# Performance work log

Hardware: AMD Instinct MI355X
Metric: run time of the kernel (lower is better)

## Reference

```python
import jax, jax.numpy as jnp
import numpy as np

NUM_EMBEDDINGS = 512
EMBEDDING_DIM = 256
COMMITMENT_COST = 0.25


def setup_inputs() -> dict:
    key = jax.random.key(0)
    k1, k2 = jax.random.split(key)
    z_e = jax.random.normal(k1, (16, EMBEDDING_DIM, 16, 16, 16), dtype=jnp.float32)
    # codebook init: uniform(-1/K, 1/K) as in the torch module
    codebook = jax.random.uniform(
        k2, (NUM_EMBEDDINGS, EMBEDDING_DIM), dtype=jnp.float32,
        minval=-1.0 / NUM_EMBEDDINGS, maxval=1.0 / NUM_EMBEDDINGS)
    return {"z_e": z_e, "codebook": codebook}


def reference(z_e, codebook):
    # z_e: [B, C, D, H, W] -> [B, D, H, W, C]
    z_p = jnp.transpose(z_e, (0, 2, 3, 4, 1))
    spatial_shape = z_p.shape[:-1]
    flat = z_p.reshape(-1, EMBEDDING_DIM)                      # [N, C]
    z_sq = jnp.sum(flat * flat, axis=1, keepdims=True)         # [N, 1]
    cb_sq = jnp.sum(codebook * codebook, axis=1)[None, :]      # [1, K]
    dot = flat @ codebook.T                                    # [N, K]
    distances = z_sq + cb_sq - 2.0 * dot
    idx = jnp.argmin(distances, axis=1)                        # [N]
    z_q_p = codebook[idx].reshape(z_p.shape)                   # [B, D, H, W, C]
    codebook_loss = jnp.mean((z_q_p - jax.lax.stop_gradient(z_p)) ** 2)
    commitment_loss = jnp.mean((z_p - jax.lax.stop_gradient(z_q_p)) ** 2)
    vq_loss = codebook_loss + COMMITMENT_COST * commitment_loss
    # straight-through estimator
    z_q_st = z_p + jax.lax.stop_gradient(z_q_p - z_p)
    z_q = jnp.transpose(z_q_st, (0, 4, 1, 2, 3))               # [B, C, D, H, W]
    encoding_indices = idx.reshape(spatial_shape)
    return z_q, vq_loss, encoding_indices
```

## Files before the change

kernel.cpp:

```cpp
#include <hip/hip_runtime.h>

#define NPOS   65536
#define CDIM   256
#define KCODES 512
#define ZTOT   16777216
#define IDX_OFF (ZTOT + 1)
#define TAU    2.0e-3f
#define GL_CAP 16384

#define WS_CBSQ 64
#define WS_CBBF 66112
#define WS_GLI  132096
#define NC_FULL 0x7fff

using bf16x8 = __attribute__((ext_vector_type(8))) short;
using f32x4  = __attribute__((ext_vector_type(4))) float;

__device__ __forceinline__ unsigned short f2bf(float f) {
    unsigned int u = __float_as_uint(f);
    return (unsigned short)((u + 0x7fffu + ((u >> 16) & 1u)) >> 16);
}

__device__ __forceinline__ float np_pw128_sq(const float* a) {
    float r[8];
    #pragma unroll
    for (int j = 0; j < 8; ++j) r[j] = __fmul_rn(a[j], a[j]);
    #pragma unroll 1
    for (int i = 8; i < 128; i += 8) {
        #pragma unroll
        for (int j = 0; j < 8; ++j)
            r[j] = __fadd_rn(r[j], __fmul_rn(a[i + j], a[i + j]));
    }
    return __fadd_rn(__fadd_rn(__fadd_rn(r[0], r[1]), __fadd_rn(r[2], r[3])),
                     __fadd_rn(__fadd_rn(r[4], r[5]), __fadd_rn(r[6], r[7])));
}

__global__ void vq_cvtprep(const float* __restrict__ cb, float* __restrict__ ws) {
    const int k = blockIdx.x;
    const int c = threadIdx.x;
    __shared__ float row[256];
    __shared__ float chres[16];
    const float v = cb[(size_t)k * CDIM + c];
    row[c] = v;
    unsigned short* cbf2 = (unsigned short*)(ws + WS_CBBF);
    const int kt = c >> 5, g = (c & 31) >> 3, j = c & 7;
    cbf2[((((k >> 4) * 8 + kt) * 64) + g * 16 + (k & 15)) * 8 + j] = f2bf(v);
    if (k == 0 && c == 0) { ws[0] = 0.0f; ((int*)ws)[1] = 0; }
    __syncthreads();
    if (c < 16) {
        const float* a = &row[(c & 8) * 16];
        const int jj = c & 7;
        float r = __fmul_rn(a[jj], a[jj]);
        #pragma unroll 1
        for (int m = 1; m < 16; ++m)
            r = __fadd_rn(r, __fmul_rn(a[jj + 8 * m], a[jj + 8 * m]));
        chres[c] = r;
    }
    __syncthreads();
    if (c == 0) {
        float h0 = __fadd_rn(__fadd_rn(__fadd_rn(chres[0], chres[1]), __fadd_rn(chres[2], chres[3])),
                             __fadd_rn(__fadd_rn(chres[4], chres[5]), __fadd_rn(chres[6], chres[7])));
        float h1 = __fadd_rn(__fadd_rn(__fadd_rn(chres[8], chres[9]), __fadd_rn(chres[10], chres[11])),
                             __fadd_rn(__fadd_rn(chres[12], chres[13]), __fadd_rn(chres[14], chres[15])));
        ws[WS_CBSQ + k] = __fadd_rn(h0, h1);
    }
}

__device__ __forceinline__ void stw(unsigned short A[2][8][64][8], int nb,
                                    int c, int q, float4 v) {
    const int kt = c >> 5, gg = (c & 31) >> 3, j = c & 7;
    unsigned short* d = &A[nb][kt][gg * 16 + q * 4][j];
    d[0]  = f2bf(v.x);
    d[8]  = f2bf(v.y);
    d[16] = f2bf(v.z);
    d[24] = f2bf(v.w);
}

__launch_bounds__(512, 2)
__global__ void vq_screen(const float* __restrict__ z,
                          float* __restrict__ ws,
                          float* __restrict__ out) {
    const int t  = threadIdx.x;
    const int w  = t >> 6;
    const int l  = t & 63;
    const int g  = l >> 4;
    const int c0 = l & 15;
    int* wsi = (int*)ws;
    const unsigned short* cbf2 = (const unsigned short*)(ws + WS_CBBF);

    __shared__ unsigned short ldsA[2][8][64][8];
    __shared__ float cbsq_s[KCODES];
    __shared__ float red_v[8][16];
    __shared__ int   red_i[8][16];
    __shared__ float fv1[16];
    __shared__ int   ccnt[16];
    __shared__ int   candk[16][8];

    cbsq_s[t] = ws[WS_CBSQ + t];
    if (t < 16) ccnt[t] = 0;

    bf16x8 bfr[4][8];
    #pragma unroll
    for (int p = 0; p < 4; ++p)
        #pragma unroll
        for (int kt = 0; kt < 8; ++kt)
            bfr[p][kt] = *(const bf16x8*)(cbf2 + ((((w * 4 + p) * 8 + kt) * 64 + l) << 3));

    const int base = blockIdx.x * 256;
    const float* zB = z + (size_t)(base >> 12) * 1048576;
    const int c1 = t >> 2, q = t & 3;

    {
        const float* zb = zB + (base & 4095);
        float4 a0 = *(const float4*)(zb + (size_t)c1 * 4096 + q * 4);
        float4 a1 = *(const float4*)(zb + (size_t)(c1 + 128) * 4096 + q * 4);
        stw(ldsA, 0, c1, q, a0);
        stw(ldsA, 0, c1 + 128, q, a1);
    }
    __syncthreads();

    #pragma unroll 1
    for (int i = 0; i < 16; ++i) {
        const int buf = i & 1;
        const int m0  = base + i * 16;

        float4 p0, p1;
        if (i < 15) {
            const float* zb = zB + ((m0 + 16) & 4095);
            p0 = *(const float4*)(zb + (size_t)c1 * 4096 + q * 4);
            p1 = *(const float4*)(zb + (size_t)(c1 + 128) * 4096 + q * 4);
        }

        f32x4 acc[4];
        #pragma unroll
        for (int p = 0; p < 4; ++p) acc[p] = (f32x4){0.f, 0.f, 0.f, 0.f};

        #pragma unroll
        for (int kt = 0; kt < 8; ++kt) {
            const bf16x8 a = *(const bf16x8*)&ldsA[buf][kt][l][0];
            acc[0] = __builtin_amdgcn_mfma_f32_16x16x32_bf16(a, bfr[0][kt], acc[0], 0, 0, 0);
            acc[1] = __builtin_amdgcn_mfma_f32_16x16x32_bf16(a, bfr[1][kt], acc[1], 0, 0, 0);
            acc[2] = __builtin_amdgcn_mfma_f32_16x16x32_bf16(a, bfr[2][kt], acc[2], 0, 0, 0);
            acc[3] = __builtin_amdgcn_mfma_f32_16x16x32_bf16(a, bfr[3][kt], acc[3], 0, 0, 0);
        }

        float v1[4]; int i1[4];
        #pragma unroll
        for (int r = 0; r < 4; ++r) { v1[r] = 3.4028235e38f; i1[r] = 0; }
        #pragma unroll
        for (int p = 0; p < 4; ++p) {
            const int k = w * 64 + p * 16 + c0;
            const float cq = cbsq_s[k];
            #pragma unroll
            for (int r = 0; r < 4; ++r) {
                const float s = fmaf(-2.0f, acc[p][r], cq);
                if (s < v1[r]) { v1[r] = s; i1[r] = k; }
            }
        }
        #pragma unroll
        for (int r = 0; r < 4; ++r) {
            #pragma unroll
            for (int m = 1; m < 16; m <<= 1) {
                float pv = __shfl_xor(v1[r], m, 64);
                int   pi = __shfl_xor(i1[r], m, 64);
                if (pv < v1[r] || (pv == v1[r] && pi < i1[r])) { v1[r] = pv; i1[r] = pi; }
            }
        }
        if (c0 == 0) {
            #pragma unroll
            for (int r = 0; r < 4; ++r) {
                red_v[w][g * 4 + r] = v1[r];
                red_i[w][g * 4 + r] = i1[r];
            }
        }
        __syncthreads();

        float gv = 0.f; int gi = 0;
        if (t < 16) {
            gv = red_v[0][t]; gi = red_i[0][t];
            #pragma unroll
            for (int ww = 1; ww < 8; ++ww) {
                const float pv = red_v[ww][t];
                const int   pi = red_i[ww][t];
                if (pv < gv || (pv == gv && pi < gi)) { gv = pv; gi = pi; }
            }
            fv1[t] = gv;
        }
        __syncthreads();

        #pragma unroll
        for (int p = 0; p < 4; ++p) {
            const int k = w * 64 + p * 16 + c0;
            const float cq = cbsq_s[k];
            #pragma unroll
            for (int r = 0; r < 4; ++r) {
                const float s = fmaf(-2.0f, acc[p][r], cq);
                const int row = g * 4 + r;
                if (s < fv1[row] + TAU) {
                    int pos = atomicAdd(&ccnt[row], 1);
                    if (pos < 8) candk[row][pos] = k;
                }
            }
        }
        if (i < 15) {
            stw(ldsA, buf ^ 1, c1, q, p0);
            stw(ldsA, buf ^ 1, c1 + 128, q, p1);
        }
        __syncthreads();

        if (t < 16) {
            const int n = m0 + t;
            out[IDX_OFF + n] = (float)gi;
            const int nc = ccnt[t];
            if (nc > 1) {
                int slot = atomicAdd(wsi + 1, 1);
                if (slot < GL_CAP) {
                    int* gl = wsi + WS_GLI + slot * 10;
                    gl[0] = n;
                    gl[1] = (nc > 8) ? NC_FULL : nc;
                    #pragma unroll
                    for (int qq = 0; qq < 8; ++qq)
                        gl[2 + qq] = (qq < nc && qq < 8) ? candk[t][qq] : 0;
                }
            }
            ccnt[t] = 0;
        }
    }
}

__global__ void vq_refine(const float* __restrict__ z,
                          const float* __restrict__ cb,
                          float* __restrict__ ws,
                          float* __restrict__ out) {
    int* wsi = (int*)ws;
    const int cnt = min(wsi[1], GL_CAP);
    const int t   = threadIdx.x;
    const int wid = t >> 6;
    const int l   = t & 63;

    __shared__ __align__(16) float zs[260];
    __shared__ float chres[16];
    __shared__ float zsq_sh;
    __shared__ float wbv[4];
    __shared__ int   wbi[4];

    for (int slot = blockIdx.x; slot < cnt; slot += gridDim.x) {
        __syncthreads();
        const int* gl = wsi + WS_GLI + slot * 10;
        const int n  = gl[0];
        const int nc = gl[1];
        const size_t zb = (size_t)(n >> 12) * 1048576 + (size_t)(n & 4095);
        zs[t] = z[zb + (size_t)t * 4096];
        __syncthreads();

        if (t < 16) {
            const float* a = &zs[(t & 8) * 16];
            const int j = t & 7;
            float r = __fmul_rn(a[j], a[j]);
            #pragma unroll 1
            for (int m = 1; m < 16; ++m)
                r = __fadd_rn(r, __fmul_rn(a[j + 8 * m], a[j + 8 * m]));
            chres[t] = r;
        }
        __syncthreads();
        if (t == 0) {
            float h0 = __fadd_rn(__fadd_rn(__fadd_rn(chres[0], chres[1]), __fadd_rn(chres[2], chres[3])),
                                 __fadd_rn(__fadd_rn(chres[4], chres[5]), __fadd_rn(chres[6], chres[7])));
            float h1 = __fadd_rn(__fadd_rn(__fadd_rn(chres[8], chres[9]), __fadd_rn(chres[10], chres[11])),
                                 __fadd_rn(__fadd_rn(chres[12], chres[13]), __fadd_rn(chres[14], chres[15])));
            zsq_sh = __fadd_rn(h0, h1);
        }
        __syncthreads();
        const float zsq = zsq_sh;
        const float4 zl = *(const float4*)&zs[4 * l];

        float bv = 3.4028235e38f;
        int   bi = 0x7fffffff;
        if (nc != NC_FULL) {
            for (int ci = wid; ci < nc; ci += 4) {
                const int k = gl[2 + ci];
                const float4 e = *(const float4*)(cb + (size_t)k * CDIM + 4 * l);
                double d = (double)e.x * (double)zl.x + (double)e.y * (double)zl.y
                         + (double)e.z * (double)zl.z + (double)e.w * (double)zl.w;
                #pragma unroll
                for (int m = 1; m < 64; m <<= 1)
                    d += __shfl_xor(d, m, 64);
                const float dist = __fsub_rn(__fadd_rn(zsq, ws[WS_CBSQ + k]),
                                             __fmul_rn(2.0f, (float)d));
                if (dist < bv || (dist == bv && k < bi)) { bv = dist; bi = k; }
            }
        } else {
            for (int k = wid; k < KCODES; k += 4) {
                const float4 e = *(const float4*)(cb + (size_t)k * CDIM + 4 * l);
                double d = (double)e.x * (double)zl.x + (double)e.y * (double)zl.y
                         + (double)e.z * (double)zl.z + (double)e.w * (double)zl.w;
                #pragma unroll
                for (int m = 1; m < 64; m <<= 1)
                    d += __shfl_xor(d, m, 64);
                const float dist = __fsub_rn(__fadd_rn(zsq, ws[WS_CBSQ + k]),
                                             __fmul_rn(2.0f, (float)d));
                if (dist < bv || (dist == bv && k < bi)) { bv = dist; bi = k; }
            }
        }
        if (l == 0) { wbv[wid] = bv; wbi[wid] = bi; }
        __syncthreads();
        if (t == 0) {
            float v = wbv[0]; int i = wbi[0];
            #pragma unroll
            for (int ww = 1; ww < 4; ++ww) {
                if (wbv[ww] < v || (wbv[ww] == v && wbi[ww] < i)) { v = wbv[ww]; i = wbi[ww]; }
            }
            out[IDX_OFF + n] = (float)i;
        }
    }
}

__launch_bounds__(256, 4)
__global__ void vq_gather(const float* __restrict__ z,
                          const float* __restrict__ cb,
                          float* __restrict__ out,
                          float* __restrict__ ws) {
    __shared__ int   sidx[32];
    __shared__ float lcb[32][257];
    const int t  = threadIdx.x;
    const int n0 = blockIdx.x * 32;
    const int b  = n0 >> 12;
    const int s0 = n0 & 4095;

    if (t < 32) sidx[t] = (int)out[IDX_OFF + n0 + t];
    __syncthreads();

    #pragma unroll 4
    for (int e = t; e < 32 * 256; e += 256) {
        const int r = e >> 8, c = e & 255;
        lcb[r][c] = cb[(size_t)sidx[r] * CDIM + c];
    }
    __syncthreads();

    float acc = 0.0f;
    const int sl = t & 31, cg = t >> 5;
    const size_t base = (size_t)b * 1048576 + (size_t)s0 + sl;
    #pragma unroll 4
    for (int i = 0; i < 32; ++i) {
        const int c = i * 8 + cg;
        const size_t o = base + (size_t)c * 4096;
        float v  = lcb[sl][c];
        float zv = z[o];
        out[o] = v;
        float df = v - zv;
        acc += df * df;
    }

    #pragma unroll
    for (int off = 32; off > 0; off >>= 1)
        acc += __shfl_down(acc, off, 64);
    __shared__ float wsum[4];
    const int lane = t & 63, wid = t >> 6;
    if (lane == 0) wsum[wid] = acc;
    __syncthreads();
    if (t == 0)
        atomicAdd(&ws[0], wsum[0] + wsum[1] + wsum[2] + wsum[3]);
}

__global__ void vq_fin(const float* __restrict__ ws, float* __restrict__ out) {
    if (threadIdx.x == 0)
        out[ZTOT] = 1.25f * ws[0] / (float)ZTOT;
}

extern "C" void kernel_launch(void* const* d_in, const int* in_sizes, int n_in,
                              void* d_out, int out_size, void* d_ws, size_t ws_size,
                              hipStream_t stream) {
    const float* z  = (const float*)d_in[0];
    const float* cb = (const float*)d_in[1];
    float* out = (float*)d_out;
    float* ws  = (float*)d_ws;

    vq_cvtprep<<<512, 256, 0, stream>>>(cb, ws);
    vq_screen<<<NPOS / 256, 512, 0, stream>>>(z, ws, out);
    vq_refine<<<2048, 256, 0, stream>>>(z, cb, ws, out);
    vq_gather<<<NPOS / 32, 256, 0, stream>>>(z, cb, out, ws);
    vq_fin<<<1, 64, 0, stream>>>(ws, out);
}
```

Baseline: 166.9 us.

## Batch screen output writes, vectorize gather stores, fold finalize into gather

```diff
diff --git a/kernel.cpp b/kernel.cpp
--- a/kernel.cpp
+++ b/kernel.cpp
@@ -45,7 +45,7 @@
     unsigned short* cbf2 = (unsigned short*)(ws + WS_CBBF);
     const int kt = c >> 5, g = (c & 31) >> 3, j = c & 7;
     cbf2[((((k >> 4) * 8 + kt) * 64) + g * 16 + (k & 15)) * 8 + j] = f2bf(v);
-    if (k == 0 && c == 0) { ws[0] = 0.0f; ((int*)ws)[1] = 0; }
+    if (k == 0 && c == 0) { ws[0] = 0.0f; ((int*)ws)[1] = 0; ((int*)ws)[2] = 0; }
     __syncthreads();
     if (c < 16) {
         const float* a = &row[(c & 8) * 16];
@@ -93,11 +93,12 @@
     __shared__ float red_v[8][16];
     __shared__ int   red_i[8][16];
     __shared__ float fv1[16];
-    __shared__ int   ccnt[16];
-    __shared__ int   candk[16][8];
+    __shared__ int   rowidx[256];
+    __shared__ int   ccnt[256];
+    __shared__ int   candk[256][8];
 
     cbsq_s[t] = ws[WS_CBSQ + t];
-    if (t < 16) ccnt[t] = 0;
+    if (t < 256) ccnt[t] = 0;
 
     bf16x8 bfr[4][8];
     #pragma unroll
@@ -120,12 +121,12 @@
     __syncthreads();
 
     #pragma unroll 1
-    for (int i = 0; i < 16; ++i) {
-        const int buf = i & 1;
-        const int m0  = base + i * 16;
+    for (int it = 0; it < 16; ++it) {
+        const int buf = it & 1;
+        const int m0  = base + it * 16;
 
         float4 p0, p1;
-        if (i < 15) {
+        if (it < 15) {
             const float* zb = zB + ((m0 + 16) & 4095);
             p0 = *(const float4*)(zb + (size_t)c1 * 4096 + q * 4);
             p1 = *(const float4*)(zb + (size_t)(c1 + 128) * 4096 + q * 4);
@@ -175,16 +176,20 @@
         }
         __syncthreads();
 
-        float gv = 0.f; int gi = 0;
-        if (t < 16) {
-            gv = red_v[0][t]; gi = red_i[0][t];
-            #pragma unroll
-            for (int ww = 1; ww < 8; ++ww) {
-                const float pv = red_v[ww][t];
-                const int   pi = red_i[ww][t];
-                if (pv < gv || (pv == gv && pi < gi)) { gv = pv; gi = pi; }
-            }
-            fv1[t] = gv;
+        if (t < 128) {
+            const int row = t >> 3, ww = t & 7;
+            float mv = red_v[ww][row];
+            int   mi = red_i[ww][row];
+            #pragma unroll
+            for (int d = 1; d < 8; d <<= 1) {
+                const float ov = __shfl_xor(mv, d, 64);
+                const int   oi = __shfl_xor(mi, d, 64);
+                if (ov < mv || (ov == mv && oi < mi)) { mv = ov; mi = oi; }
+            }
+            if (ww == 0) {
+                fv1[row] = mv;
+                rowidx[it * 16 + row] = mi;
+            }
         }
         __syncthreads();
 
@@ -197,33 +202,33 @@
                 const float s = fmaf(-2.0f, acc[p][r], cq);
                 const int row = g * 4 + r;
                 if (s < fv1[row] + TAU) {
-                    int pos = atomicAdd(&ccnt[row], 1);
-                    if (pos < 8) candk[row][pos] = k;
+                    const int grow = it * 16 + row;
+                    int pos = atomicAdd(&ccnt[grow], 1);
+                    if (pos < 8) candk[grow][pos] = k;
                 }
             }
         }
-        if (i < 15) {
+        if (it < 15) {
             stw(ldsA, buf ^ 1, c1, q, p0);
             stw(ldsA, buf ^ 1, c1 + 128, q, p1);
         }
         __syncthreads();
-
-        if (t < 16) {
-            const int n = m0 + t;
-            out[IDX_OFF + n] = (float)gi;
-            const int nc = ccnt[t];
-            if (nc > 1) {
-                int slot = atomicAdd(wsi + 1, 1);
-                if (slot < GL_CAP) {
-                    int* gl = wsi + WS_GLI + slot * 10;
-                    gl[0] = n;
-                    gl[1] = (nc > 8) ? NC_FULL : nc;
-                    #pragma unroll
-                    for (int qq = 0; qq < 8; ++qq)
-                        gl[2 + qq] = (qq < nc && qq < 8) ? candk[t][qq] : 0;
-                }
-            }
-            ccnt[t] = 0;
+    }
+
+    if (t < 256) {
+        const int n = base + t;
+        out[IDX_OFF + n] = (float)rowidx[t];
+        const int nc = ccnt[t];
+        if (nc > 1) {
+            int slot = atomicAdd(wsi + 1, 1);
+            if (slot < GL_CAP) {
+                int* gl = wsi + WS_GLI + slot * 10;
+                gl[0] = n;
+                gl[1] = (nc > 8) ? NC_FULL : nc;
+                #pragma unroll
+                for (int qq = 0; qq < 8; ++qq)
+                    gl[2 + qq] = (qq < nc && qq < 8) ? candk[t][qq] : 0;
+            }
         }
     }
 }
@@ -338,17 +343,22 @@
     __syncthreads();
 
     float acc = 0.0f;
-    const int sl = t & 31, cg = t >> 5;
-    const size_t base = (size_t)b * 1048576 + (size_t)s0 + sl;
-    #pragma unroll 4
-    for (int i = 0; i < 32; ++i) {
-        const int c = i * 8 + cg;
-        const size_t o = base + (size_t)c * 4096;
-        float v  = lcb[sl][c];
-        float zv = z[o];
-        out[o] = v;
-        float df = v - zv;
-        acc += df * df;
+    const int pq = t & 7, ch0 = t >> 3;
+    const size_t zbase = (size_t)b * 1048576 + (size_t)s0;
+    #pragma unroll
+    for (int pass = 0; pass < 8; ++pass) {
+        const int c = pass * 32 + ch0;
+        const size_t o = zbase + (size_t)c * 4096 + pq * 4;
+        const float4 zv = *(const float4*)(z + o);
+        float4 v;
+        v.x = lcb[pq * 4 + 0][c];
+        v.y = lcb[pq * 4 + 1][c];
+        v.z = lcb[pq * 4 + 2][c];
+        v.w = lcb[pq * 4 + 3][c];
+        *(float4*)(out + o) = v;
+        const float dx = v.x - zv.x, dy = v.y - zv.y;
+        const float dz = v.z - zv.z, dw = v.w - zv.w;
+        acc += dx * dx + dy * dy + dz * dz + dw * dw;
     }
 
     #pragma unroll
@@ -358,13 +368,15 @@
     const int lane = t & 63, wid = t >> 6;
     if (lane == 0) wsum[wid] = acc;
     __syncthreads();
-    if (t == 0)
+    if (t == 0) {
         atomicAdd(&ws[0], wsum[0] + wsum[1] + wsum[2] + wsum[3]);
-}
-
-__global__ void vq_fin(const float* __restrict__ ws, float* __restrict__ out) {
-    if (threadIdx.x == 0)
-        out[ZTOT] = 1.25f * ws[0] / (float)ZTOT;
+        __threadfence();
+        int ticket = atomicAdd((int*)ws + 2, 1);
+        if (ticket == (int)gridDim.x - 1) {
+            float L = atomicAdd(&ws[0], 0.0f);
+            out[ZTOT] = 1.25f * L / (float)ZTOT;
+        }
+    }
 }
 
 extern "C" void kernel_launch(void* const* d_in, const int* in_sizes, int n_in,
@@ -379,5 +391,4 @@
     vq_screen<<<NPOS / 256, 512, 0, stream>>>(z, ws, out);
     vq_refine<<<2048, 256, 0, stream>>>(z, cb, ws, out);
     vq_gather<<<NPOS / 32, 256, 0, stream>>>(z, cb, out, ws);
-    vq_fin<<<1, 64, 0, stream>>>(ws, out);
-}
+}
```

Result: slower. 229.3 us (+37.4%).
